# Kernel optimization log

Measured on AMD Instinct MI355X. Metric: run time of the kernel, lower is better.

## Reference

```python
import jax, jax.numpy as jnp
import numpy as np

B, S, H = 32, 8192, 512


def setup_inputs() -> dict:
    key = jax.random.key(0)
    k1, k2, k3, k4 = jax.random.split(key, 4)
    output = jax.random.normal(k1, (B, 1, H), dtype=jnp.float32)
    context = jax.random.normal(k2, (B, S, H), dtype=jnp.float32)
    split_index = jax.random.randint(k3, (B,), 1, S - 1)  # avoid all-masked softmax rows
    W = jax.random.normal(k4, (H, 4 * H), dtype=jnp.float32) * (1.0 / np.sqrt(4 * H))
    b = jnp.zeros((H,), dtype=jnp.float32)
    return {"output": output, "context": context, "split_index": split_index, "W": W, "b": b}


def reference(output, context, split_index, W, b):
    Bb, Ss, Hh = context.shape
    rows = jnp.arange(Bb)
    pos = jnp.arange(Ss)

    # attn = bmm(output, context^T).squeeze(1) -> [B, S]
    attn = jnp.einsum('bih,bsh->bis', output, context)[:, 0, :]
    # torch code uses attn.data (detached) for all softmax paths
    attn_d = jax.lax.stop_gradient(attn)

    # forward-side mask: positions i < split_index kept
    fmask = pos[None, :] < split_index[:, None]  # [B, S] bool
    f_logits = jnp.where(fmask, attn_d, -jnp.inf)
    f_attn = jax.nn.softmax(f_logits, axis=1)
    f_attn = f_attn.at[rows, split_index].set(0.0)  # explicit zero at split position
    a_mix = jnp.einsum('bs,bsh->bh', f_attn, context)[:, None, :]  # [B,1,H]

    # NOTE: original source has `b_attn = f_attn.view(...)` (bug), so b_mix == a_mix.
    # The b-side masked softmax is computed but dead; we replicate the realized math.
    b_mix = a_mix

    # det_att = context[b, split_index[b], :]
    det_att = context[rows, split_index][:, None, :]  # [B,1,H]

    combined = jnp.concatenate((a_mix, b_mix, det_att, output), axis=2)  # [B,1,4H]
    out = jnp.tanh(combined @ W.T + b)  # Linear(4H->H) + Tanh, [B,1,H]
    return out, attn
```

## Files before the change

### kernel.cpp

```cpp
#include <hip/hip_runtime.h>
#include <math.h>

#define BATCH 32
#define SEQ   8192
#define HID   512
#define STRIPES 16
#define RPB   (SEQ / STRIPES)
#define CR    16
#define NCHUNK (RPB / CR)

typedef float f4 __attribute__((ext_vector_type(4)));

__device__ __forceinline__ void gload_lds(const float* g, float* l) {
  __builtin_amdgcn_global_load_lds(
      (const __attribute__((address_space(1))) void*)g,
      (__attribute__((address_space(3))) void*)l, 16, 0, 0);
}

__global__ __launch_bounds__(256, 2) void k_pass1(
    const float* __restrict__ outp, const float* __restrict__ ctx,
    const int* __restrict__ split, float* __restrict__ attn_out,
    float* __restrict__ pacc, float* __restrict__ pmd)
{
  __shared__ float lds[2][CR][HID];
  const int tid = threadIdx.x, lane = tid & 63, wave = tid >> 6;
  const int b = blockIdx.x >> 4;
  const int stripe = blockIdx.x & 15;
  const int sp = split[b];
  const int s_base = stripe * RPB;

  const float* ob = outp + b * HID + lane * 8;
  const f4 o0 = *(const f4*)ob;
  const f4 o1 = *(const f4*)(ob + 4);

  const float* cbase = ctx + ((size_t)b * SEQ + s_base) * HID;
  float* ao = attn_out + (size_t)b * SEQ + s_base;

#pragma unroll
  for (int i = 0; i < 8; ++i) {
    const int o = (wave * 8 + i) * 256;
    gload_lds(cbase + o + lane * 4, &lds[0][0][0] + o);
  }

  float m = -INFINITY, d = 0.f;
  f4 acc0 = {0.f, 0.f, 0.f, 0.f}, acc1 = {0.f, 0.f, 0.f, 0.f};

  __syncthreads();

  for (int c = 0; c < NCHUNK; ++c) {
    const int cur = c & 1;
    if (c + 1 < NCHUNK) {
      const float* src = cbase + (size_t)(c + 1) * CR * HID;
      float* dst = &lds[cur ^ 1][0][0];
#pragma unroll
      for (int i = 0; i < 8; ++i) {
        const int o = (wave * 8 + i) * 256;
        gload_lds(src + o + lane * 4, dst + o);
      }
    }

    float a4[4];
#pragma unroll
    for (int k = 0; k < 4; ++k) {
      const int r = wave * 4 + k;
      const float* rp = &lds[cur][r][lane * 8];
      const f4 c0 = *(const f4*)rp;
      const f4 c1 = *(const f4*)(rp + 4);
      float v = o0[0]*c0[0] + o0[1]*c0[1] + o0[2]*c0[2] + o0[3]*c0[3]
              + o1[0]*c1[0] + o1[1]*c1[1] + o1[2]*c1[2] + o1[3]*c1[3];
#pragma unroll
      for (int off = 32; off >= 1; off >>= 1) v += __shfl_xor(v, off, 64);
      a4[k] = v;
      const int s = s_base + c * CR + r;
      if (s < sp) {
        const float nm = fmaxf(m, v);
        const float sc = __expf(m - nm);
        const float w  = __expf(v - nm);
        d = d * sc + w;
        acc0 = acc0 * sc + w * c0;
        acc1 = acc1 * sc + w * c1;
        m = nm;
      }
    }
    if (lane == 0) {
      f4 st = {a4[0], a4[1], a4[2], a4[3]};
      *(f4*)(ao + c * CR + wave * 4) = st;
    }
    __syncthreads();
  }

  float* lacc = &lds[0][0][0];
  float* lmd  = &lds[1][0][0];
  *(f4*)(lacc + wave * HID + lane * 8)     = acc0;
  *(f4*)(lacc + wave * HID + lane * 8 + 4) = acc1;
  if (lane == 0) { lmd[wave * 2] = m; lmd[wave * 2 + 1] = d; }
  __syncthreads();

  const float M = fmaxf(fmaxf(lmd[0], lmd[2]), fmaxf(lmd[4], lmd[6]));
  const size_t pb = (size_t)b * STRIPES + stripe;
  float* pa = pacc + pb * HID;
  if (M == -INFINITY) {
    pa[tid * 2] = 0.f; pa[tid * 2 + 1] = 0.f;
    if (tid == 0) { pmd[pb * 2] = -INFINITY; pmd[pb * 2 + 1] = 0.f; }
  } else {
    float e[4], Dl = 0.f;
#pragma unroll
    for (int wv = 0; wv < 4; ++wv) {
      const float mw = lmd[wv * 2];
      e[wv] = (mw == -INFINITY) ? 0.f : __expf(mw - M);
      Dl += e[wv] * lmd[wv * 2 + 1];
    }
    float s0 = 0.f, s1 = 0.f;
#pragma unroll
    for (int wv = 0; wv < 4; ++wv) {
      s0 += e[wv] * lacc[wv * HID + tid * 2];
      s1 += e[wv] * lacc[wv * HID + tid * 2 + 1];
    }
    pa[tid * 2] = s0; pa[tid * 2 + 1] = s1;
    if (tid == 0) { pmd[pb * 2] = M; pmd[pb * 2 + 1] = Dl; }
  }
}

__global__ __launch_bounds__(64) void k_final(
    const float* __restrict__ outp, const float* __restrict__ ctx,
    const int* __restrict__ split, const float* __restrict__ W,
    const float* __restrict__ bias, const float* __restrict__ pacc,
    const float* __restrict__ pmd, float* __restrict__ out0)
{
  const int b = blockIdx.x >> 3, q = blockIdx.x & 7;
  const int t = threadIdx.x;
  __shared__ float amix[HID], det[HID], oup[HID];

  float M = -INFINITY;
#pragma unroll
  for (int c = 0; c < STRIPES; ++c) M = fmaxf(M, pmd[(b * STRIPES + c) * 2]);
  float wgt[STRIPES], D = 0.f;
#pragma unroll
  for (int c = 0; c < STRIPES; ++c) {
    const float mw = pmd[(b * STRIPES + c) * 2];
    wgt[c] = (mw == -INFINITY) ? 0.f : __expf(mw - M);
    D += wgt[c] * pmd[(b * STRIPES + c) * 2 + 1];
  }
  const float invD = 1.f / D;
  const int sp = split[b];
#pragma unroll
  for (int j = 0; j < 8; ++j) {
    const int col = t * 8 + j;
    float s = 0.f;
    for (int c = 0; c < STRIPES; ++c)
      s += wgt[c] * pacc[((size_t)(b * STRIPES + c)) * HID + col];
    amix[col] = s * invD;
    det[col] = ctx[((size_t)b * SEQ + sp) * HID + col];
    oup[col] = outp[b * HID + col];
  }
  __syncthreads();

  const int h = q * 64 + t;
  float acc = bias[h];
  const float* wr = W + (size_t)h * (4 * HID);
  for (int k0 = 0; k0 < HID; k0 += 4) {
    const f4 w0 = *(const f4*)(wr + k0);
    const f4 w1 = *(const f4*)(wr + HID + k0);
    const f4 w2 = *(const f4*)(wr + 2 * HID + k0);
    const f4 w3 = *(const f4*)(wr + 3 * HID + k0);
#pragma unroll
    for (int j = 0; j < 4; ++j)
      acc += amix[k0 + j] * (w0[j] + w1[j]) + det[k0 + j] * w2[j] + oup[k0 + j] * w3[j];
  }
  out0[b * HID + h] = tanhf(acc);
}

extern "C" void kernel_launch(void* const* d_in, const int* in_sizes, int n_in,
                              void* d_out, int out_size, void* d_ws, size_t ws_size,
                              hipStream_t stream)
{
  const float* outp = (const float*)d_in[0];
  const float* ctx  = (const float*)d_in[1];
  const int*   spl  = (const int*)d_in[2];
  const float* W    = (const float*)d_in[3];
  const float* bias = (const float*)d_in[4];

  float* out0   = (float*)d_out;
  float* attn_o = out0 + (size_t)BATCH * HID;

  float* pacc = (float*)d_ws;
  float* pmd  = pacc + (size_t)BATCH * STRIPES * HID;

  k_pass1<<<BATCH * STRIPES, 256, 0, stream>>>(outp, ctx, spl, attn_o, pacc, pmd);
  k_final<<<BATCH * 8,        64, 0, stream>>>(outp, ctx, spl, W, bias, pacc, pmd, out0);
}
```

Baseline: 138.9 us.

## Use per-wave vmcnt waits with depth-2 prefetch and split final GEMV across threads

In the streaming pass, each wave only consumes the LDS rows it loaded itself. The per-chunk __syncthreads is therefore replaced by explicit s_waitcnt vmcnt/lgkmcnt waits, and the next-next chunk is prefetched into the buffer just read, giving two loads in flight. This is meant to remove block-wide barrier stalls and keep more HBM traffic in flight on a memory-bound scan. The final linear+tanh kernel now uses 256 threads, with four lanes per output each handling one quarter of the weight row, reduced by shuffles. This raises parallelism for the W read. The hand-written waitcnt counts depend on the exact number of issued loads, so any change to the load pattern could silently break correctness.

```diff
diff --git a/kernel.cpp b/kernel.cpp
--- a/kernel.cpp
+++ b/kernel.cpp
@@ -10,6 +10,11 @@
 #define NCHUNK (RPB / CR)
 
 typedef float f4 __attribute__((ext_vector_type(4)));
+
+#define VMWAIT(N) do { asm volatile("s_waitcnt vmcnt(" #N ")" ::: "memory"); \
+                       __builtin_amdgcn_sched_barrier(0); } while (0)
+#define LGKMWAIT0 do { asm volatile("s_waitcnt lgkmcnt(0)" ::: "memory"); \
+                       __builtin_amdgcn_sched_barrier(0); } while (0)
 
 __device__ __forceinline__ void gload_lds(const float* g, float* l) {
   __builtin_amdgcn_global_load_lds(
@@ -41,17 +46,34 @@
     const int o = (wave * 8 + i) * 256;
     gload_lds(cbase + o + lane * 4, &lds[0][0][0] + o);
   }
+#pragma unroll
+  for (int i = 0; i < 8; ++i) {
+    const int o = (wave * 8 + i) * 256;
+    gload_lds(cbase + CR * HID + o + lane * 4, &lds[1][0][0] + o);
+  }
 
   float m = -INFINITY, d = 0.f;
   f4 acc0 = {0.f, 0.f, 0.f, 0.f}, acc1 = {0.f, 0.f, 0.f, 0.f};
 
-  __syncthreads();
-
+#pragma unroll 1
   for (int c = 0; c < NCHUNK; ++c) {
+    if (c == 0)                 VMWAIT(8);
+    else if (c == NCHUNK - 1)   VMWAIT(1);
+    else                        VMWAIT(9);
+
     const int cur = c & 1;
-    if (c + 1 < NCHUNK) {
-      const float* src = cbase + (size_t)(c + 1) * CR * HID;
-      float* dst = &lds[cur ^ 1][0][0];
+    f4 c0[4], c1[4];
+#pragma unroll
+    for (int k = 0; k < 4; ++k) {
+      const float* rp = &lds[cur][wave * 4 + k][lane * 8];
+      c0[k] = *(const f4*)rp;
+      c1[k] = *(const f4*)(rp + 4);
+    }
+    LGKMWAIT0;
+
+    if (c + 2 < NCHUNK) {
+      const float* src = cbase + (size_t)(c + 2) * CR * HID;
+      float* dst = &lds[cur][0][0];
 #pragma unroll
       for (int i = 0; i < 8; ++i) {
         const int o = (wave * 8 + i) * 256;
@@ -62,33 +84,33 @@
     float a4[4];
 #pragma unroll
     for (int k = 0; k < 4; ++k) {
-      const int r = wave * 4 + k;
-      const float* rp = &lds[cur][r][lane * 8];
-      const f4 c0 = *(const f4*)rp;
-      const f4 c1 = *(const f4*)(rp + 4);
-      float v = o0[0]*c0[0] + o0[1]*c0[1] + o0[2]*c0[2] + o0[3]*c0[3]
-              + o1[0]*c1[0] + o1[1]*c1[1] + o1[2]*c1[2] + o1[3]*c1[3];
+      float v = o0[0]*c0[k][0] + o0[1]*c0[k][1] + o0[2]*c0[k][2] + o0[3]*c0[k][3]
+              + o1[0]*c1[k][0] + o1[1]*c1[k][1] + o1[2]*c1[k][2] + o1[3]*c1[k][3];
 #pragma unroll
       for (int off = 32; off >= 1; off >>= 1) v += __shfl_xor(v, off, 64);
       a4[k] = v;
-      const int s = s_base + c * CR + r;
+    }
+    if (lane == 0) {
+      f4 st = {a4[0], a4[1], a4[2], a4[3]};
+      *(f4*)(ao + c * CR + wave * 4) = st;
+    }
+#pragma unroll
+    for (int k = 0; k < 4; ++k) {
+      const int s = s_base + c * CR + wave * 4 + k;
       if (s < sp) {
+        const float v  = a4[k];
         const float nm = fmaxf(m, v);
         const float sc = __expf(m - nm);
         const float w  = __expf(v - nm);
         d = d * sc + w;
-        acc0 = acc0 * sc + w * c0;
-        acc1 = acc1 * sc + w * c1;
+        acc0 = acc0 * sc + w * c0[k];
+        acc1 = acc1 * sc + w * c1[k];
         m = nm;
       }
     }
-    if (lane == 0) {
-      f4 st = {a4[0], a4[1], a4[2], a4[3]};
-      *(f4*)(ao + c * CR + wave * 4) = st;
-    }
-    __syncthreads();
-  }
-
+  }
+
+  __syncthreads();
   float* lacc = &lds[0][0][0];
   float* lmd  = &lds[1][0][0];
   *(f4*)(lacc + wave * HID + lane * 8)     = acc0;
@@ -121,15 +143,18 @@
   }
 }
 
-__global__ __launch_bounds__(64) void k_final(
+__global__ __launch_bounds__(256) void k_final(
     const float* __restrict__ outp, const float* __restrict__ ctx,
     const int* __restrict__ split, const float* __restrict__ W,
     const float* __restrict__ bias, const float* __restrict__ pacc,
     const float* __restrict__ pmd, float* __restrict__ out0)
 {
   const int b = blockIdx.x >> 3, q = blockIdx.x & 7;
-  const int t = threadIdx.x;
-  __shared__ float amix[HID], det[HID], oup[HID];
+  const int tid = threadIdx.x;
+  __shared__ float comb[3 * HID + 8];
+  float* amixp = comb;
+  float* detp  = comb + HID + 4;
+  float* oupp  = comb + 2 * HID + 8;
 
   float M = -INFINITY;
 #pragma unroll
@@ -144,30 +169,31 @@
   const float invD = 1.f / D;
   const int sp = split[b];
 #pragma unroll
-  for (int j = 0; j < 8; ++j) {
-    const int col = t * 8 + j;
+  for (int col = tid; col < HID; col += 256) {
     float s = 0.f;
+#pragma unroll
     for (int c = 0; c < STRIPES; ++c)
       s += wgt[c] * pacc[((size_t)(b * STRIPES + c)) * HID + col];
-    amix[col] = s * invD;
-    det[col] = ctx[((size_t)b * SEQ + sp) * HID + col];
-    oup[col] = outp[b * HID + col];
+    amixp[col] = s * invD;
+    detp[col]  = ctx[((size_t)b * SEQ + sp) * HID + col];
+    oupp[col]  = outp[b * HID + col];
   }
   __syncthreads();
 
-  const int h = q * 64 + t;
-  float acc = bias[h];
-  const float* wr = W + (size_t)h * (4 * HID);
+  const int hl = tid >> 2, part = tid & 3;
+  const int h = q * 64 + hl;
+  const float* wr = W + (size_t)h * (4 * HID) + part * HID;
+  const float* src = (part == 2) ? detp : (part == 3 ? oupp : amixp);
+  float acc = 0.f;
+#pragma unroll 4
   for (int k0 = 0; k0 < HID; k0 += 4) {
-    const f4 w0 = *(const f4*)(wr + k0);
-    const f4 w1 = *(const f4*)(wr + HID + k0);
-    const f4 w2 = *(const f4*)(wr + 2 * HID + k0);
-    const f4 w3 = *(const f4*)(wr + 3 * HID + k0);
-#pragma unroll
-    for (int j = 0; j < 4; ++j)
-      acc += amix[k0 + j] * (w0[j] + w1[j]) + det[k0 + j] * w2[j] + oup[k0 + j] * w3[j];
-  }
-  out0[b * HID + h] = tanhf(acc);
+    const f4 w = *(const f4*)(wr + k0);
+    const f4 x = *(const f4*)(src + k0);
+    acc += w[0]*x[0] + w[1]*x[1] + w[2]*x[2] + w[3]*x[3];
+  }
+  acc += __shfl_xor(acc, 1, 64);
+  acc += __shfl_xor(acc, 2, 64);
+  if (part == 0) out0[b * HID + h] = tanhf(acc + bias[h]);
 }
 
 extern "C" void kernel_launch(void* const* d_in, const int* in_sizes, int n_in,
@@ -187,5 +213,5 @@
   float* pmd  = pacc + (size_t)BATCH * STRIPES * HID;
 
   k_pass1<<<BATCH * STRIPES, 256, 0, stream>>>(outp, ctx, spl, attn_o, pacc, pmd);
-  k_final<<<BATCH * 8,        64, 0, stream>>>(outp, ctx, spl, W, bias, pacc, pmd, out0);
-}
+  k_final<<<BATCH * 8,       256, 0, stream>>>(outp, ctx, spl, W, bias, pacc, pmd, out0);
+}
```

After: 122.9 us (median of 2 runs). 11.5% less time.
